# Optimization experiments

Measured on AMD Instinct MI355X. Metric: run time of the kernel, lower is better.

Reference implementation:

```python
import jax, jax.numpy as jnp
import numpy as np

IN_FEATURES = 1024
OUT_FEATURES = 256
NUM_KNOTS = 10
SPLINE_ORDER = 3
NUM_BASIS = NUM_KNOTS + SPLINE_ORDER  # 13
EPS = 1e-8


def setup_inputs() -> dict:
    key = jax.random.key(0)
    k1, k2 = jax.random.split(key)
    x = jax.random.normal(k1, (8192, IN_FEATURES), dtype=jnp.float32)
    spline_coeffs = jax.random.normal(
        k2, (OUT_FEATURES, IN_FEATURES, NUM_BASIS), dtype=jnp.float32) * 0.1
    knots = jnp.linspace(-1.0, 1.0, NUM_KNOTS + 2 * SPLINE_ORDER, dtype=jnp.float32)
    return {"x": x, "spline_coeffs": spline_coeffs, "knots": knots}


def _basis_functions(x, knots):
    # x: (B, I) already tanh-normalized; returns (B, I, NUM_BASIS)
    xc = jnp.clip(x, -1.0, 1.0)[..., None]          # (B, I, 1)
    left = knots[:NUM_BASIS - 1]                     # (nb-1,)
    center = knots[1:NUM_BASIS]                      # (nb-1,)
    right = knots[2:NUM_BASIS + 1]                   # (nb-1,)  (i+2 < len(knots) always)
    mask_l = (xc >= left) & (xc < center)
    mask_r = (xc >= center) & (xc < right)
    up = mask_l.astype(xc.dtype) * (xc - left) / (center - left + EPS)
    down = mask_r.astype(xc.dtype) * (right - xc) / (right - center + EPS)
    b = up + down                                    # (B, I, nb-1)
    # last basis column is never written in the original loop -> zeros
    return jnp.pad(b, ((0, 0), (0, 0), (0, 1)))


def reference(x, spline_coeffs, knots):
    x_norm = jnp.tanh(x)
    basis = _basis_functions(x_norm, knots)          # (B, I, K)
    # output[b, j] = sum_i sum_k basis[b, i, k] * coeffs[j, i, k]
    return jnp.einsum('bik,jik->bj', basis, spline_coeffs)
```

## Files before the change

kernel.cpp:

```cpp
#include <hip/hip_runtime.h>
#include <cstdint>
#include <cstddef>


typedef _Float16 half2_v __attribute__((ext_vector_type(2)));
typedef __fp16  fp16x2  __attribute__((ext_vector_type(2)));
typedef _Float16 f16x8 __attribute__((ext_vector_type(8)));
typedef float f32x4 __attribute__((ext_vector_type(4)));

__device__ __forceinline__ half2_v u32_as_h2(uint32_t u) {
  union { uint32_t u; half2_v h; } c; c.u = u; return c.h;
}
__device__ __forceinline__ uint32_t h2_as_u32(half2_v h) {
  union { uint32_t u; half2_v h; } c; c.h = h; return c.u;
}
__device__ __forceinline__ half2_v cvt_pk_h2(float a, float b) {
  union { fp16x2 f; half2_v h; } c;
  c.f = __builtin_amdgcn_cvt_pkrtz(a, b);
  return c.h;
}
__device__ __forceinline__ float dot2f(half2_v a, half2_v b, float c) {
#if __has_builtin(__builtin_amdgcn_fdot2)
  return __builtin_amdgcn_fdot2(a, b, c, false);
#else
  return c + (float)a[0] * (float)b[0] + (float)a[1] * (float)b[1];
#endif
}
__device__ __forceinline__ uint16_t f16_bits(float v) {
  union { _Float16 h; uint16_t u; } c; c.h = (_Float16)v; return c.u;
}

__device__ __forceinline__ float fast_tanhf(float v) {
  const float e = __expf(2.0f * v);
  return 1.0f - 2.0f / (e + 1.0f);
}

#define KSTEP 0.13333333333333333f
#define KINV  7.49999943750004f
__device__ __forceinline__ void kan_weights(float xin, float& w0, float& w1, int& lo) {
  float xc = fast_tanhf(xin);
  xc = fminf(fmaxf(xc, -1.0f), 1.0f);
  int m = (int)((xc + 1.0f) * 7.5f);
  m = min(max(m, 0), 14);
  const float k0 = fmaf((float)m, KSTEP, -1.0f);
  const float up = (xc - k0) * KINV;
  const float dn = (k0 + KSTEP - xc) * KINV;
  w0 = (m == 0) ? up : ((m <= 12) ? dn : 0.0f);
  w1 = (m >= 1 && m <= 11) ? up : 0.0f;
  lo = min(max(m - 1, 0), 11);
}

__device__ __forceinline__ void load_lds16(const void* g, void* l) {
  __builtin_amdgcn_global_load_lds((const __attribute__((address_space(1))) void*)g,
                                   (__attribute__((address_space(3))) void*)l, 16, 0, 0);
}

#define GMM 8192
#define GNN 256
#define KI  12
#define GK2 (1024 * KI)
#define KSPL2 8
#define IPER (1024 / KSPL2)
#define BM2 128
#define BN2 256
#define NSG 16
#define NSTEP 48
#define AS_STRIDE 208
#define AS_SG (128 * AS_STRIDE)

__global__ __launch_bounds__(256)
void kan_prep_B2(const float* __restrict__ coef, uint32_t* __restrict__ B2,
                 float4* __restrict__ outz) {
  const int tid = blockIdx.x * 256 + threadIdx.x;
  const float* cp = coef + (size_t)tid * 13;
  uint32_t w[6];
#pragma unroll
  for (int q = 0; q < 6; ++q) w[q] = h2_as_u32(cvt_pk_h2(cp[2 * q], cp[2 * q + 1]));
  uint2* p = (uint2*)(B2 + (size_t)tid * 6);
  p[0] = make_uint2(w[0], w[1]);
  p[1] = make_uint2(w[2], w[3]);
  p[2] = make_uint2(w[4], w[5]);
  const float4 z = make_float4(0.f, 0.f, 0.f, 0.f);
  outz[tid] = z;
  outz[tid + 262144] = z;
}

__global__ __launch_bounds__(512, 2)
void kan_gemm12(const float* __restrict__ x, const _Float16* __restrict__ B2,
                float* __restrict__ out) {
  __shared__ __align__(16) char Bs[4][16384];
  __shared__ __align__(16) char As[2][AS_SG];
  char* BsP = (char*)Bs;
  char* AsP = (char*)As;

  const int t    = threadIdx.x;
  const int lane = t & 63;
  const int wv   = t >> 6;
  const int wm   = (wv & 1) * 64;
  const int wn   = (wv >> 1) * 64;
  const int fr   = lane & 15;
  const int fq   = lane >> 4;
  const int m0   = blockIdx.z * BM2;
  const int i00  = blockIdx.x * IPER;

  const int a_base = (wm + fr) * AS_STRIDE + fq * 16;
  const int b_base = (wn + fr) * 64 + ((fq ^ (fr & 3)) * 16);

  f32x4 acc[4][4];
#pragma unroll
  for (int a = 0; a < 4; ++a)
#pragma unroll
    for (int b = 0; b < 4; ++b) acc[a][b] = (f32x4){0.f, 0.f, 0.f, 0.f};

  const int srow0 = t >> 2, sc0 = t & 3;
  const int srow1 = 128 + (t >> 2);
  const _Float16* sp0 = B2 + (size_t)srow0 * GK2 + (size_t)i00 * KI
                        + ((sc0 ^ (srow0 & 3)) * 8);
  const _Float16* sp1 = B2 + (size_t)srow1 * GK2 + (size_t)i00 * KI
                        + ((sc0 ^ (srow1 & 3)) * 8);

  const int xrow  = t & 127;
  const int i_loc = t >> 7;
  const float* xptr = x + (size_t)(m0 + xrow) * 1024 + i00 + i_loc;

  auto expand1 = [&](int dst, float xv, int il) {
    float w0, w1; int lo;
    kan_weights(xv, w0, w1, lo);
    const uint32_t wp  = (uint32_t)f16_bits(w0) | ((uint32_t)f16_bits(w1) << 16);
    const uint32_t wlo = (lo & 1) ? (wp << 16) : wp;
    const uint32_t whi = (lo & 1) ? (wp >> 16) : 0u;
    const int w   = lo >> 1;
    const int wn1 = (w + 1 > 5) ? 5 : (w + 1);
    char* rb = AsP + dst + xrow * AS_STRIDE + il * 24;
    if ((il & 1) == 0) {
      *(uint4*)(rb)      = make_uint4(0u, 0u, 0u, 0u);
      *(uint2*)(rb + 16) = make_uint2(0u, 0u);
    } else {
      *(uint2*)(rb)      = make_uint2(0u, 0u);
      *(uint4*)(rb + 8)  = make_uint4(0u, 0u, 0u, 0u);
    }
    *(uint32_t*)(rb + wn1 * 4) = whi;
    *(uint32_t*)(rb + w * 4)   = wlo;
  };

  float cxa, cxb, nxa = 0.f, nxb = 0.f;

  {
    const float exa = xptr[0];
    const float exb = xptr[4];
    load_lds16(sp0, BsP + t * 16);
    load_lds16(sp1, BsP + 8192 + t * 16);
    sp0 += 32; sp1 += 32;
    load_lds16(sp0, BsP + 16384 + t * 16);
    load_lds16(sp1, BsP + 16384 + 8192 + t * 16);
    sp0 += 32; sp1 += 32;
    expand1(0, exa, i_loc);
    expand1(0, exb, i_loc + 4);
    cxa = xptr[8];
    cxb = xptr[12];
  }
  asm volatile("s_waitcnt vmcnt(2) lgkmcnt(0)" ::: "memory");
  __builtin_amdgcn_s_barrier();
  __builtin_amdgcn_sched_barrier(0);

#define GRANP(U, PH, XPF)                                                     \
  {                                                                           \
    const int g = 12 * B + 3 * (U) + (PH);                                    \
    const char* Asrc = AsP + ((U) & 1) * AS_SG;                               \
    f16x8 af0 = *(const f16x8*)(Asrc + a_base + (PH) * 64);                   \
    f16x8 af1 = *(const f16x8*)(Asrc + a_base + (PH) * 64 + 16 * AS_STRIDE);  \
    f16x8 af2 = *(const f16x8*)(Asrc + a_base + (PH) * 64 + 32 * AS_STRIDE);  \
    f16x8 af3 = *(const f16x8*)(Asrc + a_base + (PH) * 64 + 48 * AS_STRIDE);  \
    load_lds16(sp0, BsP + ((3 * (U) + (PH) + 2) & 3) * 16384 + t * 16);       \
    load_lds16(sp1, BsP + ((3 * (U) + (PH) + 2) & 3) * 16384 + 8192 + t * 16);\
    { const int adv = (g + 3 <= NSTEP - 1) ? 32 : 0; sp0 += adv; sp1 += adv; }\
    XPF                                                                       \
    if ((PH) == 0 && (4 * B + (U)) < NSG - 1)                                 \
      expand1((((U) + 1) & 1) * AS_SG, cxa, i_loc);                           \
    if ((PH) == 1 && (4 * B + (U)) < NSG - 1)                                 \
      expand1((((U) + 1) & 1) * AS_SG, cxb, i_loc + 4);                       \
    asm volatile("s_waitcnt vmcnt(3) lgkmcnt(0)" ::: "memory");               \
    __builtin_amdgcn_s_barrier();                                             \
    __builtin_amdgcn_sched_barrier(0);                                        \
    __builtin_amdgcn_s_setprio(1);                                            \
    _Pragma("unroll")                                                         \
    for (int ni = 0; ni < 4; ++ni) {                                          \
      const f16x8 bf = *(const f16x8*)(BsP + ((3 * (U) + (PH)) & 3) * 16384   \
                                       + b_base + ni * 1024);                 \
      acc[0][ni] = __builtin_amdgcn_mfma_f32_16x16x32_f16(af0, bf, acc[0][ni], 0, 0, 0); \
      acc[1][ni] = __builtin_amdgcn_mfma_f32_16x16x32_f16(af1, bf, acc[1][ni], 0, 0, 0); \
      acc[2][ni] = __builtin_amdgcn_mfma_f32_16x16x32_f16(af2, bf, acc[2][ni], 0, 0, 0); \
      acc[3][ni] = __builtin_amdgcn_mfma_f32_16x16x32_f16(af3, bf, acc[3][ni], 0, 0, 0); \
    }                                                                         \
    __builtin_amdgcn_s_setprio(0);                                            \
  }

#define SGBODY(U)                                                             \
  {                                                                           \
    const int sgp = 4 * B + (U) + 2;                                          \
    const int sgn = (sgp < NSG) ? sgp : (NSG - 1);                            \
    GRANP(U, 0, { nxa = xptr[8 * sgn]; })                                     \
    GRANP(U, 1, { })                                                          \
    GRANP(U, 2, { nxb = xptr[8 * sgn + 4]; })                                 \
    cxa = nxa; cxb = nxb;                                                     \
  }

  for (int B = 0; B < 4; ++B) {
    SGBODY(0)
    SGBODY(1)
    SGBODY(2)
    SGBODY(3)
  }
#undef SGBODY
#undef GRANP

#pragma unroll
  for (int q = 0; q < 4; ++q) {
    const int gr = m0 + wm + q * 16 + fq * 4;
#pragma unroll
    for (int ni = 0; ni < 4; ++ni) {
      const int gc = wn + ni * 16 + fr;
#pragma unroll
      for (int r = 0; r < 4; ++r)
        atomicAdd(&out[(size_t)(gr + r) * GNN + gc], acc[q][ni][r]);
    }
  }
}

#define TI 8
#define BT 256
#define JT 32
#define ISPL 2
#define IRANGE (1024 / ISPL)

__global__ __launch_bounds__(256)
void kan_dot2(const float* __restrict__ x, const float* __restrict__ coef,
              float* __restrict__ out) {
  __shared__ uint32_t Plds[TI * 12 * JT];
  const int t    = threadIdx.x;
  const int b    = blockIdx.x * BT + t;
  const int j0   = blockIdx.y * JT;
  const int cbeg = blockIdx.z * (IRANGE / TI);

  float acc[JT];
#pragma unroll
  for (int q = 0; q < JT; ++q) acc[q] = 0.0f;

  const int s_jj   = t & 31;
  const int s_iloc = t >> 5;

  for (int c = cbeg; c < cbeg + IRANGE / TI; ++c) {
    const int i0 = c * TI;
    __syncthreads();
    {
      const float* cp0 = coef + ((size_t)(j0 + s_jj) * 1024 + (i0 + s_iloc)) * 13;
      float cv[13];
#pragma unroll
      for (int s = 0; s < 13; ++s) cv[s] = cp0[s];
#pragma unroll
      for (int r = 0; r < 12; ++r) {
        half2_v h; h[0] = (_Float16)cv[r]; h[1] = (_Float16)cv[r + 1];
        const int slot = ((s_jj >> 2) + r) & 7;
        Plds[(s_iloc * 12 + r) * 32 + slot * 4 + (s_jj & 3)] = h2_as_u32(h);
      }
    }
    uint32_t wr[TI]; int lor[TI];
    {
      const float* xr = x + (size_t)b * 1024 + i0;
      const float4 xa = *(const float4*)(xr);
      const float4 xb = *(const float4*)(xr + 4);
      const float xv[TI] = {xa.x, xa.y, xa.z, xa.w, xb.x, xb.y, xb.z, xb.w};
#pragma unroll
      for (int q = 0; q < TI; ++q) {
        float w0, w1; int lo;
        kan_weights(xv[q], w0, w1, lo);
        wr[q] = (uint32_t)f16_bits(w0) | ((uint32_t)f16_bits(w1) << 16);
        lor[q] = lo;
      }
    }
    __syncthreads();

    const uint4* P4 = (const uint4*)Plds;
#pragma unroll
    for (int ii = 0; ii < TI; ++ii) {
      const half2_v hw = u32_as_h2(wr[ii]);
      const int lo = lor[ii];
      const int base = (ii * 12 + lo) * 8;
#pragma unroll
      for (int g = 0; g < 8; ++g) {
        const uint4 v = P4[base + ((g + lo) & 7)];
        acc[4 * g + 0] = dot2f(hw, u32_as_h2(v.x), acc[4 * g + 0]);
        acc[4 * g + 1] = dot2f(hw, u32_as_h2(v.y), acc[4 * g + 1]);
        acc[4 * g + 2] = dot2f(hw, u32_as_h2(v.z), acc[4 * g + 2]);
        acc[4 * g + 3] = dot2f(hw, u32_as_h2(v.w), acc[4 * g + 3]);
      }
    }
  }

  float* orow = out + (size_t)b * 256 + j0;
#pragma unroll
  for (int q = 0; q < JT; ++q) atomicAdd(orow + q, acc[q]);
}

extern "C" void kernel_launch(void* const* d_in, const int* in_sizes, int n_in,
                              void* d_out, int out_size, void* d_ws, size_t ws_size,
                              hipStream_t stream) {
  const float* x     = (const float*)d_in[0];
  const float* coef  = (const float*)d_in[1];
  float* out = (float*)d_out;

  const size_t nB2 = (size_t)GNN * GK2;
  if (ws_size >= nB2 * 2) {
    _Float16* B2 = (_Float16*)d_ws;
    kan_prep_B2<<<(int)((size_t)GNN * 1024 / 256), 256, 0, stream>>>(
        coef, (uint32_t*)B2, (float4*)out);
    dim3 grid(KSPL2, 1, GMM / BM2);
    kan_gemm12<<<grid, 512, 0, stream>>>(x, B2, out);
  } else {
    (void)hipMemsetAsync(out, 0, (size_t)out_size * sizeof(float), stream);
    dim3 grid(8192 / BT, 256 / JT, ISPL);
    kan_dot2<<<grid, 256, 0, stream>>>(x, coef, out);
  }
}
```

Measured before the change: 196.4 us.

## Shrink M tile, reduce split-K to two, replace atomics with partial-sum reduction

Changes the GEMM tiling from 128-row tiles with 8-way K split to 64-row tiles with 2-way K split, so each block iterates four times as many K steps with half the accumulators. Output accumulation switches from fp32 atomicAdd into a zeroed output to plain stores into two partial buffers in workspace, followed by a separate reduce kernel. This removes atomic traffic and output zeroing. It costs an extra kernel launch, more workspace traffic, and lower MFMA reuse per loaded B tile, since the B operand is now shared across fewer rows.

```diff
diff --git a/kernel.cpp b/kernel.cpp
--- a/kernel.cpp
+++ b/kernel.cpp
@@ -59,18 +59,19 @@
 #define GNN 256
 #define KI  12
 #define GK2 (1024 * KI)
-#define KSPL2 8
+#define KSPL2 2
 #define IPER (1024 / KSPL2)
-#define BM2 128
+#define BM2 64
 #define BN2 256
-#define NSG 16
-#define NSTEP 48
+#define NSG 64
+#define NSTEP 192
 #define AS_STRIDE 208
-#define AS_SG (128 * AS_STRIDE)
+#define AS_SG (64 * AS_STRIDE)
+#define OUT_ELEMS (8192 * 256)
 
 __global__ __launch_bounds__(256)
 void kan_prep_B2(const float* __restrict__ coef, uint32_t* __restrict__ B2,
-                 float4* __restrict__ outz) {
+                 float4* __restrict__ outz, int zero_out) {
   const int tid = blockIdx.x * 256 + threadIdx.x;
   const float* cp = coef + (size_t)tid * 13;
   uint32_t w[6];
@@ -80,14 +81,25 @@
   p[0] = make_uint2(w[0], w[1]);
   p[1] = make_uint2(w[2], w[3]);
   p[2] = make_uint2(w[4], w[5]);
-  const float4 z = make_float4(0.f, 0.f, 0.f, 0.f);
-  outz[tid] = z;
-  outz[tid + 262144] = z;
+  if (zero_out) {
+    const float4 z = make_float4(0.f, 0.f, 0.f, 0.f);
+    outz[tid] = z;
+    outz[tid + 262144] = z;
+  }
+}
+
+__global__ __launch_bounds__(256)
+void kan_reduce2(const float4* __restrict__ part, float4* __restrict__ out) {
+  const int i = blockIdx.x * 256 + threadIdx.x;
+  out[i] = make_float4(part[i].x + part[i + OUT_ELEMS / 4].x,
+                       part[i].y + part[i + OUT_ELEMS / 4].y,
+                       part[i].z + part[i + OUT_ELEMS / 4].z,
+                       part[i].w + part[i + OUT_ELEMS / 4].w);
 }
 
 __global__ __launch_bounds__(512, 2)
-void kan_gemm12(const float* __restrict__ x, const _Float16* __restrict__ B2,
-                float* __restrict__ out) {
+void kan_gemm13(const float* __restrict__ x, const _Float16* __restrict__ B2,
+                float* __restrict__ out, float* __restrict__ part, int mode) {
   __shared__ __align__(16) char Bs[4][16384];
   __shared__ __align__(16) char As[2][AS_SG];
   char* BsP = (char*)Bs;
@@ -96,7 +108,7 @@
   const int t    = threadIdx.x;
   const int lane = t & 63;
   const int wv   = t >> 6;
-  const int wm   = (wv & 1) * 64;
+  const int wm   = (wv & 1) * 32;
   const int wn   = (wv >> 1) * 64;
   const int fr   = lane & 15;
   const int fq   = lane >> 4;
@@ -106,9 +118,9 @@
   const int a_base = (wm + fr) * AS_STRIDE + fq * 16;
   const int b_base = (wn + fr) * 64 + ((fq ^ (fr & 3)) * 16);
 
-  f32x4 acc[4][4];
-#pragma unroll
-  for (int a = 0; a < 4; ++a)
+  f32x4 acc[2][4];
+#pragma unroll
+  for (int a = 0; a < 2; ++a)
 #pragma unroll
     for (int b = 0; b < 4; ++b) acc[a][b] = (f32x4){0.f, 0.f, 0.f, 0.f};
 
@@ -119,11 +131,12 @@
   const _Float16* sp1 = B2 + (size_t)srow1 * GK2 + (size_t)i00 * KI
                         + ((sc0 ^ (srow1 & 3)) * 8);
 
-  const int xrow  = t & 127;
-  const int i_loc = t >> 7;
+  const int xrow  = t & 63;
+  const int i_loc = t >> 6;
   const float* xptr = x + (size_t)(m0 + xrow) * 1024 + i00 + i_loc;
-
-  auto expand1 = [&](int dst, float xv, int il) {
+  const int exp_off = xrow * AS_STRIDE + i_loc * 24;
+
+  auto expand1 = [&](int dst, float xv) {
     float w0, w1; int lo;
     kan_weights(xv, w0, w1, lo);
     const uint32_t wp  = (uint32_t)f16_bits(w0) | ((uint32_t)f16_bits(w1) << 16);
@@ -131,8 +144,8 @@
     const uint32_t whi = (lo & 1) ? (wp >> 16) : 0u;
     const int w   = lo >> 1;
     const int wn1 = (w + 1 > 5) ? 5 : (w + 1);
-    char* rb = AsP + dst + xrow * AS_STRIDE + il * 24;
-    if ((il & 1) == 0) {
+    char* rb = AsP + dst + exp_off;
+    if ((i_loc & 1) == 0) {
       *(uint4*)(rb)      = make_uint4(0u, 0u, 0u, 0u);
       *(uint2*)(rb + 16) = make_uint2(0u, 0u);
     } else {
@@ -143,21 +156,18 @@
     *(uint32_t*)(rb + w * 4)   = wlo;
   };
 
-  float cxa, cxb, nxa = 0.f, nxb = 0.f;
+  float cx, nx = 0.f;
 
   {
-    const float exa = xptr[0];
-    const float exb = xptr[4];
+    const float ex = xptr[0];
     load_lds16(sp0, BsP + t * 16);
     load_lds16(sp1, BsP + 8192 + t * 16);
     sp0 += 32; sp1 += 32;
     load_lds16(sp0, BsP + 16384 + t * 16);
     load_lds16(sp1, BsP + 16384 + 8192 + t * 16);
     sp0 += 32; sp1 += 32;
-    expand1(0, exa, i_loc);
-    expand1(0, exb, i_loc + 4);
-    cxa = xptr[8];
-    cxb = xptr[12];
+    expand1(0, ex);
+    cx = xptr[8];
   }
   asm volatile("s_waitcnt vmcnt(2) lgkmcnt(0)" ::: "memory");
   __builtin_amdgcn_s_barrier();
@@ -169,16 +179,12 @@
     const char* Asrc = AsP + ((U) & 1) * AS_SG;                               \
     f16x8 af0 = *(const f16x8*)(Asrc + a_base + (PH) * 64);                   \
     f16x8 af1 = *(const f16x8*)(Asrc + a_base + (PH) * 64 + 16 * AS_STRIDE);  \
-    f16x8 af2 = *(const f16x8*)(Asrc + a_base + (PH) * 64 + 32 * AS_STRIDE);  \
-    f16x8 af3 = *(const f16x8*)(Asrc + a_base + (PH) * 64 + 48 * AS_STRIDE);  \
     load_lds16(sp0, BsP + ((3 * (U) + (PH) + 2) & 3) * 16384 + t * 16);       \
     load_lds16(sp1, BsP + ((3 * (U) + (PH) + 2) & 3) * 16384 + 8192 + t * 16);\
     { const int adv = (g + 3 <= NSTEP - 1) ? 32 : 0; sp0 += adv; sp1 += adv; }\
     XPF                                                                       \
     if ((PH) == 0 && (4 * B + (U)) < NSG - 1)                                 \
-      expand1((((U) + 1) & 1) * AS_SG, cxa, i_loc);                           \
-    if ((PH) == 1 && (4 * B + (U)) < NSG - 1)                                 \
-      expand1((((U) + 1) & 1) * AS_SG, cxb, i_loc + 4);                       \
+      expand1((((U) + 1) & 1) * AS_SG, cx);                                   \
     asm volatile("s_waitcnt vmcnt(3) lgkmcnt(0)" ::: "memory");               \
     __builtin_amdgcn_s_barrier();                                             \
     __builtin_amdgcn_sched_barrier(0);                                        \
@@ -189,8 +195,6 @@
                                        + b_base + ni * 1024);                 \
       acc[0][ni] = __builtin_amdgcn_mfma_f32_16x16x32_f16(af0, bf, acc[0][ni], 0, 0, 0); \
       acc[1][ni] = __builtin_amdgcn_mfma_f32_16x16x32_f16(af1, bf, acc[1][ni], 0, 0, 0); \
-      acc[2][ni] = __builtin_amdgcn_mfma_f32_16x16x32_f16(af2, bf, acc[2][ni], 0, 0, 0); \
-      acc[3][ni] = __builtin_amdgcn_mfma_f32_16x16x32_f16(af3, bf, acc[3][ni], 0, 0, 0); \
     }                                                                         \
     __builtin_amdgcn_s_setprio(0);                                            \
   }
@@ -199,13 +203,13 @@
   {                                                                           \
     const int sgp = 4 * B + (U) + 2;                                          \
     const int sgn = (sgp < NSG) ? sgp : (NSG - 1);                            \
-    GRANP(U, 0, { nxa = xptr[8 * sgn]; })                                     \
-    GRANP(U, 1, { })                                                          \
-    GRANP(U, 2, { nxb = xptr[8 * sgn + 4]; })                                 \
-    cxa = nxa; cxb = nxb;                                                     \
-  }
-
-  for (int B = 0; B < 4; ++B) {
+    GRANP(U, 0, { })                                                          \
+    GRANP(U, 1, { nx = xptr[8 * sgn]; })                                      \
+    GRANP(U, 2, { })                                                          \
+    cx = nx;                                                                  \
+  }
+
+  for (int B = 0; B < 16; ++B) {
     SGBODY(0)
     SGBODY(1)
     SGBODY(2)
@@ -214,15 +218,30 @@
 #undef SGBODY
 #undef GRANP
 
-#pragma unroll
-  for (int q = 0; q < 4; ++q) {
-    const int gr = m0 + wm + q * 16 + fq * 4;
-#pragma unroll
-    for (int ni = 0; ni < 4; ++ni) {
-      const int gc = wn + ni * 16 + fr;
-#pragma unroll
-      for (int r = 0; r < 4; ++r)
-        atomicAdd(&out[(size_t)(gr + r) * GNN + gc], acc[q][ni][r]);
+  if (mode) {
+    float* pb = part + (size_t)blockIdx.x * OUT_ELEMS;
+#pragma unroll
+    for (int q = 0; q < 2; ++q) {
+      const int gr = m0 + wm + q * 16 + fq * 4;
+#pragma unroll
+      for (int ni = 0; ni < 4; ++ni) {
+        const int gc = wn + ni * 16 + fr;
+#pragma unroll
+        for (int r = 0; r < 4; ++r)
+          pb[(size_t)(gr + r) * GNN + gc] = acc[q][ni][r];
+      }
+    }
+  } else {
+#pragma unroll
+    for (int q = 0; q < 2; ++q) {
+      const int gr = m0 + wm + q * 16 + fq * 4;
+#pragma unroll
+      for (int ni = 0; ni < 4; ++ni) {
+        const int gc = wn + ni * 16 + fr;
+#pragma unroll
+        for (int r = 0; r < 4; ++r)
+          atomicAdd(&out[(size_t)(gr + r) * GNN + gc], acc[q][ni][r]);
+      }
     }
   }
 }
@@ -309,13 +328,23 @@
   const float* coef  = (const float*)d_in[1];
   float* out = (float*)d_out;
 
-  const size_t nB2 = (size_t)GNN * GK2;
-  if (ws_size >= nB2 * 2) {
+  const size_t b2_bytes   = (size_t)GNN * GK2 * 2;
+  const size_t part_off   = b2_bytes;
+  const size_t part_bytes = (size_t)KSPL2 * OUT_ELEMS * 4;
+
+  if (ws_size >= part_off + part_bytes) {
     _Float16* B2 = (_Float16*)d_ws;
-    kan_prep_B2<<<(int)((size_t)GNN * 1024 / 256), 256, 0, stream>>>(
-        coef, (uint32_t*)B2, (float4*)out);
+    float* part  = (float*)((char*)d_ws + part_off);
+    kan_prep_B2<<<1024, 256, 0, stream>>>(coef, (uint32_t*)B2, (float4*)out, 0);
     dim3 grid(KSPL2, 1, GMM / BM2);
-    kan_gemm12<<<grid, 512, 0, stream>>>(x, B2, out);
+    kan_gemm13<<<grid, 512, 0, stream>>>(x, B2, out, part, 1);
+    kan_reduce2<<<OUT_ELEMS / 4 / 256, 256, 0, stream>>>((const float4*)part,
+                                                         (float4*)out);
+  } else if (ws_size >= b2_bytes) {
+    _Float16* B2 = (_Float16*)d_ws;
+    kan_prep_B2<<<1024, 256, 0, stream>>>(coef, (uint32_t*)B2, (float4*)out, 1);
+    dim3 grid(KSPL2, 1, GMM / BM2);
+    kan_gemm13<<<grid, 512, 0, stream>>>(x, B2, out, nullptr, 0);
   } else {
     (void)hipMemsetAsync(out, 0, (size_t)out_size * sizeof(float), stream);
     dim3 grid(8192 / BT, 256 / JT, ISPL);
```

New measurement: 187.5 us. 1.05x faster.

## Halve K-split and replace atomic accumulation with partial buffers plus reduce kernel

Applied to the files above, without the earlier changes.

The K dimension is now split into 4 chunks instead of 8, so each block runs twice as many subgroups, and the LDS row stride for A is changed. When the workspace is large enough, each K-split block writes plain stores into its own partial output slice, and a separate kernel sums the four slices into the output. This removes the float atomics and the zero-fill of the output. In exchange it adds a 32 MB partial-buffer write and read plus an extra launch, and halves the grid to 256 blocks.

```diff
diff --git a/kernel.cpp b/kernel.cpp
--- a/kernel.cpp
+++ b/kernel.cpp
@@ -59,18 +59,19 @@
 #define GNN 256
 #define KI  12
 #define GK2 (1024 * KI)
-#define KSPL2 8
+#define KSPL2 4
 #define IPER (1024 / KSPL2)
 #define BM2 128
 #define BN2 256
-#define NSG 16
-#define NSTEP 48
-#define AS_STRIDE 208
+#define NSG 32
+#define NSTEP 96
+#define AS_STRIDE 200
 #define AS_SG (128 * AS_STRIDE)
+#define OUT_ELEMS (8192 * 256)
 
 __global__ __launch_bounds__(256)
 void kan_prep_B2(const float* __restrict__ coef, uint32_t* __restrict__ B2,
-                 float4* __restrict__ outz) {
+                 float4* __restrict__ outz, int zero_out) {
   const int tid = blockIdx.x * 256 + threadIdx.x;
   const float* cp = coef + (size_t)tid * 13;
   uint32_t w[6];
@@ -80,14 +81,27 @@
   p[0] = make_uint2(w[0], w[1]);
   p[1] = make_uint2(w[2], w[3]);
   p[2] = make_uint2(w[4], w[5]);
-  const float4 z = make_float4(0.f, 0.f, 0.f, 0.f);
-  outz[tid] = z;
-  outz[tid + 262144] = z;
+  if (zero_out) {
+    const float4 z = make_float4(0.f, 0.f, 0.f, 0.f);
+    outz[tid] = z;
+    outz[tid + 262144] = z;
+  }
+}
+
+__global__ __launch_bounds__(256)
+void kan_reduce4(const float4* __restrict__ part, float4* __restrict__ out) {
+  const int i = blockIdx.x * 256 + threadIdx.x;
+  const float4 a = part[i];
+  const float4 b = part[i + OUT_ELEMS / 4];
+  const float4 c = part[i + 2 * (OUT_ELEMS / 4)];
+  const float4 d = part[i + 3 * (OUT_ELEMS / 4)];
+  out[i] = make_float4(a.x + b.x + c.x + d.x, a.y + b.y + c.y + d.y,
+                       a.z + b.z + c.z + d.z, a.w + b.w + c.w + d.w);
 }
 
 __global__ __launch_bounds__(512, 2)
-void kan_gemm12(const float* __restrict__ x, const _Float16* __restrict__ B2,
-                float* __restrict__ out) {
+void kan_gemm15(const float* __restrict__ x, const _Float16* __restrict__ B2,
+                float* __restrict__ out, float* __restrict__ part, int mode) {
   __shared__ __align__(16) char Bs[4][16384];
   __shared__ __align__(16) char As[2][AS_SG];
   char* BsP = (char*)Bs;
@@ -205,7 +219,7 @@
     cxa = nxa; cxb = nxb;                                                     \
   }
 
-  for (int B = 0; B < 4; ++B) {
+  for (int B = 0; B < 8; ++B) {
     SGBODY(0)
     SGBODY(1)
     SGBODY(2)
@@ -214,15 +228,30 @@
 #undef SGBODY
 #undef GRANP
 
-#pragma unroll
-  for (int q = 0; q < 4; ++q) {
-    const int gr = m0 + wm + q * 16 + fq * 4;
-#pragma unroll
-    for (int ni = 0; ni < 4; ++ni) {
-      const int gc = wn + ni * 16 + fr;
-#pragma unroll
-      for (int r = 0; r < 4; ++r)
-        atomicAdd(&out[(size_t)(gr + r) * GNN + gc], acc[q][ni][r]);
+  if (mode) {
+    float* pb = part + (size_t)blockIdx.x * OUT_ELEMS;
+#pragma unroll
+    for (int q = 0; q < 4; ++q) {
+      const int gr = m0 + wm + q * 16 + fq * 4;
+#pragma unroll
+      for (int ni = 0; ni < 4; ++ni) {
+        const int gc = wn + ni * 16 + fr;
+#pragma unroll
+        for (int r = 0; r < 4; ++r)
+          pb[(size_t)(gr + r) * GNN + gc] = acc[q][ni][r];
+      }
+    }
+  } else {
+#pragma unroll
+    for (int q = 0; q < 4; ++q) {
+      const int gr = m0 + wm + q * 16 + fq * 4;
+#pragma unroll
+      for (int ni = 0; ni < 4; ++ni) {
+        const int gc = wn + ni * 16 + fr;
+#pragma unroll
+        for (int r = 0; r < 4; ++r)
+          atomicAdd(&out[(size_t)(gr + r) * GNN + gc], acc[q][ni][r]);
+      }
     }
   }
 }
@@ -309,13 +338,23 @@
   const float* coef  = (const float*)d_in[1];
   float* out = (float*)d_out;
 
-  const size_t nB2 = (size_t)GNN * GK2;
-  if (ws_size >= nB2 * 2) {
+  const size_t b2_bytes   = (size_t)GNN * GK2 * 2;
+  const size_t part_off   = b2_bytes;
+  const size_t part_bytes = (size_t)KSPL2 * OUT_ELEMS * 4;
+
+  if (ws_size >= part_off + part_bytes) {
     _Float16* B2 = (_Float16*)d_ws;
-    kan_prep_B2<<<(int)((size_t)GNN * 1024 / 256), 256, 0, stream>>>(
-        coef, (uint32_t*)B2, (float4*)out);
+    float* part  = (float*)((char*)d_ws + part_off);
+    kan_prep_B2<<<1024, 256, 0, stream>>>(coef, (uint32_t*)B2, (float4*)out, 0);
     dim3 grid(KSPL2, 1, GMM / BM2);
-    kan_gemm12<<<grid, 512, 0, stream>>>(x, B2, out);
+    kan_gemm15<<<grid, 512, 0, stream>>>(x, B2, out, part, 1);
+    kan_reduce4<<<OUT_ELEMS / 4 / 256, 256, 0, stream>>>((const float4*)part,
+                                                         (float4*)out);
+  } else if (ws_size >= b2_bytes) {
+    _Float16* B2 = (_Float16*)d_ws;
+    kan_prep_B2<<<1024, 256, 0, stream>>>(coef, (uint32_t*)B2, (float4*)out, 1);
+    dim3 grid(KSPL2, 1, GMM / BM2);
+    kan_gemm15<<<grid, 512, 0, stream>>>(x, B2, out, nullptr, 0);
   } else {
     (void)hipMemsetAsync(out, 0, (size_t)out_size * sizeof(float), stream);
     dim3 grid(8192 / BT, 256 / JT, ISPL);
```

New measurement: 217.4 us. +10.7%, slower.
